# Kernel tuning notes

Measured on AMD Instinct MI355X. Metric: run time of the kernel, lower is better.

## Reference

```python
import jax, jax.numpy as jnp
import numpy as np

N_NODES = 100000
N_EDGES = 8192
DEG = 32                      # nodes per hyperedge
NNZ = N_EDGES * DEG
D_IN = 128
D_HID = 128
D_EDGE = 64
EPS = 1e-5


def _batchnorm(x, g, b):
    # normalize per-feature over the batch (dim 0), as a BatchNorm1d in train mode
    mu = jnp.mean(x, axis=0)
    var = jnp.var(x, axis=0)
    return (x - mu) * jax.lax.rsqrt(var + EPS) * g + b


def _hconv(x, src, eid, w, W, b):
    # hypergraph conv: linear -> node->edge weighted sum -> edge->node weighted sum
    h = x @ W + b                                          # [N, Dout]
    m = jax.ops.segment_sum(w[:, None] * h[src], eid, num_segments=N_EDGES)
    out = jax.ops.segment_sum(w[:, None] * m[eid], src, num_segments=N_NODES)
    return out


def setup_inputs() -> dict:
    key = jax.random.key(0)
    ks = jax.random.split(key, 20)
    src = jax.random.randint(ks[0], (NNZ,), 0, N_NODES)
    eid = jnp.arange(NNZ) // DEG                          # every edge id appears DEG times
    edge_index = jnp.stack([src, eid]).astype(jnp.int64)
    s = lambda k, sh, f: jax.random.normal(k, sh, jnp.float32) * f
    return {
        "x": s(ks[1], (N_NODES, D_IN), 1.0),
        "edge_index": edge_index,
        "edge_weight": jax.random.uniform(ks[2], (NNZ,), jnp.float32),
        "edge_features": s(ks[3], (N_EDGES, D_EDGE), 1.0),
        "adj": jax.random.uniform(ks[4], (N_EDGES, N_EDGES), jnp.float32) / N_EDGES,
        "T": 2,
        "norm1_g": jnp.ones((D_IN,), jnp.float32),
        "norm1_b": jnp.zeros((D_IN,), jnp.float32),
        "norm2_g": jnp.ones((D_EDGE,), jnp.float32),
        "norm2_b": jnp.zeros((D_EDGE,), jnp.float32),
        "W1": s(ks[5], (D_IN, D_HID), 0.05),
        "b1": jnp.zeros((D_HID,), jnp.float32),
        "W2": s(ks[6], (D_HID, D_HID), 0.05),
        "b2": jnp.zeros((D_HID,), jnp.float32),
        "Wn": s(ks[7], (D_HID, D_HID), 0.05),
        "We": s(ks[8], (D_EDGE, D_HID), 0.05),
        "Wg": s(ks[9], (D_HID, D_HID), 0.05),
        "cls_w1": s(ks[10], (D_HID, 16), 0.1),
        "cls_b1": jnp.zeros((16,), jnp.float32),
        "cls_w2": s(ks[11], (16, 2), 0.1),
        "cls_b2": jnp.zeros((2,), jnp.float32),
    }


def reference(x, edge_index, edge_weight, edge_features, adj, T,
              norm1_g, norm1_b, norm2_g, norm2_b,
              W1, b1, W2, b2, Wn, We, Wg,
              cls_w1, cls_b1, cls_w2, cls_b2):
    src, eid = edge_index[0], edge_index[1]
    x = _batchnorm(x, norm1_g, norm1_b)
    x = _hconv(x, src, eid, edge_weight, W1, b1)
    x = _hconv(x, src, eid, edge_weight, W2, b2)
    x = jax.nn.relu(x)
    # aggregate_node_features (mean over nodes incident to each hyperedge) —
    # the per-edge Python loop becomes one fused segment reduce
    s = jax.ops.segment_sum(x[src], eid, num_segments=N_EDGES)           # [E, D]
    cnt = jax.ops.segment_sum(jnp.ones_like(eid, jnp.float32), eid, num_segments=N_EDGES)
    node_features = s / jnp.maximum(cnt, 1.0)[:, None]
    ef = _batchnorm(edge_features, norm2_g, norm2_b)
    # edge-level graph convolution with T propagation steps over edge-edge adj
    h = jax.nn.relu(node_features @ Wn + ef @ We)
    for _ in range(T):
        h = jax.nn.relu(adj @ (h @ Wg))
    # classifier head
    out = jax.nn.relu(h @ cls_w1 + cls_b1) @ cls_w2 + cls_b2             # [E, 2]
    return out
```

## Files before the change

### kernel.cpp

```cpp
#include <hip/hip_runtime.h>

#define N_NODESC 100000
#define N_EDGESC 8192
#define DEGC 32
#define DF 128
#define DEF 64
#define EPSV 1e-5f
#define KSPLIT 8
#define KSLICE (N_EDGESC / KSPLIT)

typedef __attribute__((ext_vector_type(8))) short short8;
typedef __attribute__((ext_vector_type(4))) float f32x4;
typedef __attribute__((ext_vector_type(8))) unsigned short ushort8;
typedef __attribute__((ext_vector_type(4))) unsigned short u16x4;

typedef const void __attribute__((address_space(1)))* gptr_t;
typedef void __attribute__((address_space(3)))* lptr_t;

__device__ __forceinline__ unsigned short f2bf(float x) {
    union { float f; unsigned u; } v; v.f = x;
    unsigned r = v.u + 0x7fffu + ((v.u >> 16) & 1u);
    return (unsigned short)(r >> 16);
}

template<int DCOL, int RP>
__global__ __launch_bounds__(256) void colstats(const float* __restrict__ X, long nrows,
                                                float* __restrict__ stats) {
    const int f = threadIdx.x % DCOL;
    const int rg = threadIdx.x / DCOL;
    float s = 0.f, s2 = 0.f;
    for (long r = (long)blockIdx.x * RP + rg; r < nrows; r += (long)gridDim.x * RP) {
        float v = X[r * DCOL + f];
        s += v; s2 += v * v;
    }
    __shared__ float l1[256], l2[256];
    l1[threadIdx.x] = s; l2[threadIdx.x] = s2;
    __syncthreads();
    if (threadIdx.x < DCOL) {
        for (int g = 1; g < RP; ++g) { s += l1[threadIdx.x + g * DCOL]; s2 += l2[threadIdx.x + g * DCOL]; }
        atomicAdd(&stats[f], s);
        atomicAdd(&stats[DCOL + f], s2);
    }
}

__global__ void finalize_both(const float* __restrict__ stats,
                              const float* __restrict__ g1, const float* __restrict__ b1,
                              const float* __restrict__ g2, const float* __restrict__ b2,
                              float* __restrict__ ssx, float* __restrict__ sse) {
    int t = threadIdx.x;
    if (t < 128) {
        float mean = stats[t] / (float)N_NODESC;
        float var = stats[128 + t] / (float)N_NODESC - mean * mean;
        float sc = g1[t] * rsqrtf(var + EPSV);
        ssx[t] = sc;
        ssx[128 + t] = b1[t] - mean * sc;
    } else {
        int f = t - 128;
        float mean = stats[512 + f] / (float)N_EDGESC;
        float var = stats[576 + f] / (float)N_EDGESC - mean * mean;
        float sc = g2[f] * rsqrtf(var + EPSV);
        sse[f] = sc;
        sse[64 + f] = b2[f] - mean * sc;
    }
}

__global__ __launch_bounds__(256) void csr_fill(const int* __restrict__ src,
                                                const float* __restrict__ ew,
                                                int* __restrict__ cnt,
                                                int* __restrict__ se,
                                                float* __restrict__ swt) {
    int i = blockIdx.x * 256 + threadIdx.x;
    int n = src[i];
    int pos = atomicAdd(&cnt[n], 1);
    if (pos < DEGC) {
        se[(size_t)n * DEGC + pos] = i >> 5;
        swt[(size_t)n * DEGC + pos] = ew[i];
    }
}

__global__ __launch_bounds__(256) void node_apply(const float* __restrict__ m,
                                                  const int* __restrict__ cnt,
                                                  const int* __restrict__ se,
                                                  const float* __restrict__ swt,
                                                  float* __restrict__ out) {
    const int n = blockIdx.x * 2 + (threadIdx.x >> 7);
    const int f = threadIdx.x & 127;
    if (n >= N_NODESC) return;
    int d = cnt[n];
    if (d <= 0) return;
    d = min(d, DEGC);
    const size_t base = (size_t)n * DEGC;
    float acc = 0.f;
    for (int p = 0; p < d; ++p) {
        int e = se[base + p];
        float w = swt[base + p];
        acc += w * m[(size_t)e * DF + f];
    }
    out[(size_t)n * DF + f] = acc;
}

template<bool WEIGHTED, bool AFFINE, bool RELU, bool WRITE_SW>
__global__ __launch_bounds__(128) void gather_k(const float* __restrict__ X,
                                                const float* __restrict__ w,
                                                const int* __restrict__ src,
                                                const float* __restrict__ scale,
                                                const float* __restrict__ shift,
                                                float* __restrict__ out,
                                                float* __restrict__ swout,
                                                float mul) {
    const int e = blockIdx.x, f = threadIdx.x;
    const int base = e * DEGC;
    float acc = 0.f, sw = 0.f;
    #pragma unroll
    for (int j = 0; j < DEGC; ++j) {
        int n = src[base + j];
        float wj = WEIGHTED ? w[base + j] : 1.f;
        float v = X[(size_t)n * DF + f];
        if (RELU) v = fmaxf(v, 0.f);
        acc += wj * v;
        sw += wj;
    }
    float r = acc;
    if (AFFINE) r = acc * scale[f] + sw * shift[f];
    out[(size_t)e * DF + f] = r * mul;
    if (WRITE_SW && f == 0) swout[e] = sw;
}

template<int K1, int K2, int NSLICE, bool RELU_IN, bool RELU_OUT, bool BIAS, bool TBF16>
__global__ __launch_bounds__(256) void egemm(const float* __restrict__ A1, const float* __restrict__ W1p,
                                             const float* __restrict__ A2, const float* __restrict__ W2p,
                                             const float* __restrict__ sc2, const float* __restrict__ sh2,
                                             const float* __restrict__ bias, const float* __restrict__ swv,
                                             float* __restrict__ C, unsigned short* __restrict__ Ct) {
    constexpr int K2c = (K2 > 0) ? K2 : 1;
    constexpr size_t SLSTR = (size_t)N_EDGESC * K1;
    __shared__ float wt1[DF * K1];
    __shared__ float a1c[32 * K1];
    __shared__ float wt2[(K2 > 0) ? DF * K2c : 1];
    __shared__ float a2c[(K2 > 0) ? 32 * K2c : 1];

    const int tid = threadIdx.x;
    const int r0 = blockIdx.x * 32;

    for (int idx = tid; idx < K1 * DF; idx += 256) {
        int k = idx >> 7, c = idx & 127;
        int pc = (k >> 2) ^ ((c >> 3) & 7);
        wt1[c * K1 + pc * 4 + (k & 3)] = W1p[idx];
    }
    for (int idx = tid; idx < 32 * K1; idx += 256) {
        float v;
        if constexpr (NSLICE > 1) {
            v = 0.f;
            #pragma unroll
            for (int s = 0; s < NSLICE; ++s) v += A1[s * SLSTR + (size_t)r0 * K1 + idx];
        } else {
            v = A1[(size_t)r0 * K1 + idx];
        }
        if (RELU_IN) v = fmaxf(v, 0.f);
        a1c[idx] = v;
    }
    if constexpr (K2 > 0) {
        for (int idx = tid; idx < K2 * DF; idx += 256) {
            int k = idx >> 7, c = idx & 127;
            int pc = (k >> 2) ^ ((c >> 3) & 7);
            wt2[c * K2c + pc * 4 + (k & 3)] = W2p[idx];
        }
        for (int idx = tid; idx < 32 * K2; idx += 256) {
            int k = idx % K2;
            a2c[idx] = A2[(size_t)r0 * K2 + idx] * sc2[k] + sh2[k];
        }
    }
    __syncthreads();

    const int cg = tid & 31, rg = tid >> 5;
    const int swz = (cg >> 1) & 7;
    float acc[4][4];
    if constexpr (BIAS) {
        float bl[4], sl[4];
        #pragma unroll
        for (int j = 0; j < 4; ++j) bl[j] = bias[cg * 4 + j];
        #pragma unroll
        for (int i = 0; i < 4; ++i) sl[i] = swv[r0 + rg * 4 + i];
        #pragma unroll
        for (int i = 0; i < 4; ++i)
            #pragma unroll
            for (int j = 0; j < 4; ++j) acc[i][j] = sl[i] * bl[j];
    } else {
        #pragma unroll
        for (int i = 0; i < 4; ++i)
            #pragma unroll
            for (int j = 0; j < 4; ++j) acc[i][j] = 0.f;
    }

    #pragma unroll 4
    for (int k4 = 0; k4 < K1; k4 += 4) {
        f32x4 av[4], wv[4];
        const int pk = (((k4 >> 2) ^ swz) << 2);
        #pragma unroll
        for (int i = 0; i < 4; ++i) av[i] = *(const f32x4*)&a1c[(rg * 4 + i) * K1 + k4];
        #pragma unroll
        for (int j = 0; j < 4; ++j) wv[j] = *(const f32x4*)&wt1[(cg * 4 + j) * K1 + pk];
        #pragma unroll
        for (int i = 0; i < 4; ++i)
            #pragma unroll
            for (int j = 0; j < 4; ++j)
                #pragma unroll
                for (int q = 0; q < 4; ++q) acc[i][j] += av[i][q] * wv[j][q];
    }
    if constexpr (K2 > 0) {
        #pragma unroll 4
        for (int k4 = 0; k4 < K2; k4 += 4) {
            f32x4 av[4], wv[4];
            const int pk = (((k4 >> 2) ^ swz) << 2);
            #pragma unroll
            for (int i = 0; i < 4; ++i) av[i] = *(const f32x4*)&a2c[(rg * 4 + i) * K2c + k4];
            #pragma unroll
            for (int j = 0; j < 4; ++j) wv[j] = *(const f32x4*)&wt2[(cg * 4 + j) * K2c + pk];
            #pragma unroll
            for (int i = 0; i < 4; ++i)
                #pragma unroll
                for (int j = 0; j < 4; ++j)
                    #pragma unroll
                    for (int q = 0; q < 4; ++q) acc[i][j] += av[i][q] * wv[j][q];
        }
    }

    if constexpr (TBF16) {
        #pragma unroll
        for (int j = 0; j < 4; ++j) {
            u16x4 o;
            #pragma unroll
            for (int i = 0; i < 4; ++i) {
                float v = acc[i][j];
                if (RELU_OUT) v = fmaxf(v, 0.f);
                o[i] = f2bf(v);
            }
            *(u16x4*)&Ct[(size_t)(cg * 4 + j) * N_EDGESC + r0 + rg * 4] = o;
        }
    } else {
        #pragma unroll
        for (int i = 0; i < 4; ++i) {
            f32x4 o;
            #pragma unroll
            for (int j = 0; j < 4; ++j) {
                float v = acc[i][j];
                if (RELU_OUT) v = fmaxf(v, 0.f);
                o[j] = v;
            }
            *(f32x4*)&C[(size_t)(r0 + rg * 4 + i) * DF + cg * 4] = o;
        }
    }
}

template<bool CVT>
__global__ __launch_bounds__(256, 2) void adj_gemm(const unsigned short* __restrict__ Abf,
                                                   const float* __restrict__ Af32,
                                                   unsigned short* __restrict__ Aout,
                                                   const unsigned short* __restrict__ Bt,
                                                   float* __restrict__ H) {
    __shared__ unsigned short sA[2][128 * 64];
    __shared__ unsigned short sB[2][128 * 64];
    const int tid = threadIdx.x;
    const int lane = tid & 63, wave = tid >> 6;
    const int mb = blockIdx.x & 63, ks = blockIdx.x >> 6;
    const size_t m0 = (size_t)mb * 128;
    const int k0 = ks * KSLICE;
    const int wm = wave >> 1, wn = wave & 1;
    float* __restrict__ Hs = H + (size_t)ks * (N_EDGESC * DF);

    f32x4 acc[4][4];
    #pragma unroll
    for (int i = 0; i < 4; ++i)
        #pragma unroll
        for (int j = 0; j < 4; ++j) acc[i][j] = 0.f;

    auto stage = [&](int buf, int kc) {
        #pragma unroll
        for (int i = 0; i < 4; ++i) {
            int slot = i * 256 + wave * 64 + lane;
            int row = slot >> 3, ch = slot & 7;
            int sc = (ch ^ (row & 7)) << 3;
            if constexpr (CVT) {
                const float* ga = Af32 + (m0 + row) * (size_t)N_EDGESC + kc + sc;
                f32x4 a = *(const f32x4*)ga;
                f32x4 b = *(const f32x4*)(ga + 4);
                ushort8 r;
                r[0] = f2bf(a[0]); r[1] = f2bf(a[1]); r[2] = f2bf(a[2]); r[3] = f2bf(a[3]);
                r[4] = f2bf(b[0]); r[5] = f2bf(b[1]); r[6] = f2bf(b[2]); r[7] = f2bf(b[3]);
                *(ushort8*)&sA[buf][slot * 8] = r;
                *(ushort8*)(Aout + (m0 + row) * (size_t)N_EDGESC + kc + sc) = r;
            } else {
                const unsigned short* ga = Abf + (m0 + row) * (size_t)N_EDGESC + kc + sc;
                unsigned short* la = &sA[buf][(i * 256 + wave * 64) * 8];
                __builtin_amdgcn_global_load_lds((gptr_t)ga, (lptr_t)la, 16, 0, 0);
            }
            const unsigned short* gb = Bt + (size_t)row * N_EDGESC + kc + sc;
            unsigned short* lb = &sB[buf][(i * 256 + wave * 64) * 8];
            __builtin_amdgcn_global_load_lds((gptr_t)gb, (lptr_t)lb, 16, 0, 0);
        }
    };

    stage(0, k0);
    int cur = 0;
    for (int c = 0; c < KSLICE / 64; ++c) {
        __syncthreads();
        if (c + 1 < KSLICE / 64) stage(cur ^ 1, k0 + (c + 1) * 64);
        #pragma unroll
        for (int kk = 0; kk < 2; ++kk) {
            short8 af[4], bv[4];
            const int chb = kk * 4 + (lane >> 4);
            #pragma unroll
            for (int mf = 0; mf < 4; ++mf) {
                int row = wm * 64 + mf * 16 + (lane & 15);
                af[mf] = *(const short8*)&sA[cur][(row * 8 + (chb ^ (row & 7))) * 8];
            }
            #pragma unroll
            for (int nf = 0; nf < 4; ++nf) {
                int row = wn * 64 + nf * 16 + (lane & 15);
                bv[nf] = *(const short8*)&sB[cur][(row * 8 + (chb ^ (row & 7))) * 8];
            }
            #pragma unroll
            for (int mf = 0; mf < 4; ++mf)
                #pragma unroll
                for (int nf = 0; nf < 4; ++nf)
                    acc[mf][nf] = __builtin_amdgcn_mfma_f32_16x16x32_bf16(af[mf], bv[nf], acc[mf][nf], 0, 0, 0);
        }
        cur ^= 1;
    }

    #pragma unroll
    for (int mf = 0; mf < 4; ++mf)
        #pragma unroll
        for (int nf = 0; nf < 4; ++nf)
            #pragma unroll
            for (int r = 0; r < 4; ++r) {
                size_t row = m0 + wm * 64 + mf * 16 + (lane >> 4) * 4 + r;
                int col = wn * 64 + nf * 16 + (lane & 15);
                Hs[row * DF + col] = acc[mf][nf][r];
            }
}

__global__ __launch_bounds__(256) void classifier_k(const float* __restrict__ H,
                                                    const float* __restrict__ w1, const float* __restrict__ b1,
                                                    const float* __restrict__ w2, const float* __restrict__ b2,
                                                    float* __restrict__ out) {
    constexpr size_t SLSTR = (size_t)N_EDGESC * DF;
    __shared__ float hl[16 * DF];
    __shared__ float w1l[DF * 16];
    __shared__ float hid[16 * 16];
    const int tid = threadIdx.x;
    const int e0 = blockIdx.x * 16;
    for (int idx = tid; idx < 16 * DF; idx += 256) {
        float v = 0.f;
        #pragma unroll
        for (int s = 0; s < KSPLIT; ++s) v += H[s * SLSTR + (size_t)e0 * DF + idx];
        hl[idx] = fmaxf(v, 0.f);
    }
    for (int idx = tid; idx < DF * 16; idx += 256) w1l[idx] = w1[idx];
    __syncthreads();
    {
        int el = tid >> 4, j = tid & 15;
        float a = b1[j];
        for (int k = 0; k < DF; ++k) a += hl[el * DF + k] * w1l[k * 16 + j];
        hid[el * 16 + j] = fmaxf(a, 0.f);
    }
    __syncthreads();
    if (tid < 32) {
        int e = tid >> 1, o = tid & 1;
        float s = b2[o];
        for (int jj = 0; jj < 16; ++jj) s += hid[e * 16 + jj] * w2[jj * 2 + o];
        out[(size_t)(e0 + e) * 2 + o] = s;
    }
}

extern "C" void kernel_launch(void* const* d_in, const int* in_sizes, int n_in,
                              void* d_out, int out_size, void* d_ws, size_t ws_size,
                              hipStream_t stream) {
    const float* x   = (const float*)d_in[0];
    const int*  src  = (const int*)d_in[1];
    const float* ew  = (const float*)d_in[2];
    const float* ef  = (const float*)d_in[3];
    const float* adj = (const float*)d_in[4];
    const float* n1g = (const float*)d_in[6];
    const float* n1b = (const float*)d_in[7];
    const float* n2g = (const float*)d_in[8];
    const float* n2b = (const float*)d_in[9];
    const float* W1  = (const float*)d_in[10];
    const float* b1  = (const float*)d_in[11];
    const float* W2  = (const float*)d_in[12];
    const float* b2  = (const float*)d_in[13];
    const float* Wn  = (const float*)d_in[14];
    const float* We  = (const float*)d_in[15];
    const float* Wg  = (const float*)d_in[16];
    const float* cw1 = (const float*)d_in[17];
    const float* cb1 = (const float*)d_in[18];
    const float* cw2 = (const float*)d_in[19];
    const float* cb2 = (const float*)d_in[20];
    float* out = (float*)d_out;

    float* stats  = (float*)d_ws;
    float* ssx    = stats + 256;
    float* sse    = stats + 640;
    float* sw     = stats + 1024;
    int*   cnt    = (int*)(sw + 8192);
    int*   se     = cnt + N_NODESC;
    float* swt    = (float*)(se + (size_t)N_NODESC * DEGC);
    float* EB0    = swt + (size_t)N_NODESC * DEGC;
    float* EB1    = EB0 + (size_t)N_EDGESC * DF;
    float* HS     = EB1 + (size_t)N_EDGESC * DF;
    float* NODES  = HS + (size_t)KSPLIT * N_EDGESC * DF;
    unsigned short* yT    = (unsigned short*)(NODES + (size_t)N_NODESC * DF);
    unsigned short* adjbf = yT + (size_t)DF * N_EDGESC;

    (void)hipMemsetAsync(stats, 0, (1024 + 8192) * sizeof(float) + N_NODESC * sizeof(int), stream);

    colstats<128, 2><<<400, 256, 0, stream>>>(x, N_NODESC, stats);
    colstats<64, 4><<<64, 256, 0, stream>>>(ef, N_EDGESC, stats + 512);
    finalize_both<<<1, 192, 0, stream>>>(stats, n1g, n1b, n2g, n2b, ssx, sse);

    csr_fill<<<(N_EDGESC * DEGC) / 256, 256, 0, stream>>>(src, ew, cnt, se, swt);

    gather_k<true, true, false, true><<<N_EDGESC, 128, 0, stream>>>(x, ew, src, ssx, ssx + 128, EB0, sw, 1.f);
    egemm<128, 0, 1, false, false, true, false><<<256, 256, 0, stream>>>(EB0, W1, nullptr, nullptr, nullptr, nullptr, b1, sw, EB1, nullptr);
    node_apply<<<N_NODESC / 2, 256, 0, stream>>>(EB1, cnt, se, swt, NODES);

    gather_k<true, false, false, false><<<N_EDGESC, 128, 0, stream>>>(NODES, ew, src, nullptr, nullptr, EB0, nullptr, 1.f);
    egemm<128, 0, 1, false, false, true, false><<<256, 256, 0, stream>>>(EB0, W2, nullptr, nullptr, nullptr, nullptr, b2, sw, EB1, nullptr);
    node_apply<<<N_NODESC / 2, 256, 0, stream>>>(EB1, cnt, se, swt, NODES);

    gather_k<false, false, true, false><<<N_EDGESC, 128, 0, stream>>>(NODES, nullptr, src, nullptr, nullptr, EB0, nullptr, 1.f / DEGC);

    egemm<128, 64, 1, false, true, false, false><<<256, 256, 0, stream>>>(EB0, Wn, ef, We, sse, sse + 64, nullptr, nullptr, EB1, nullptr);

    egemm<128, 0, 1, false, false, false, true><<<256, 256, 0, stream>>>(EB1, Wg, nullptr, nullptr, nullptr, nullptr, nullptr, nullptr, nullptr, yT);
    adj_gemm<true><<<64 * KSPLIT, 256, 0, stream>>>(nullptr, adj, adjbf, yT, HS);
    egemm<128, 0, KSPLIT, true, false, false, true><<<256, 256, 0, stream>>>(HS, Wg, nullptr, nullptr, nullptr, nullptr, nullptr, nullptr, nullptr, yT);
    adj_gemm<false><<<64 * KSPLIT, 256, 0, stream>>>(adjbf, nullptr, nullptr, yT, HS);

    classifier_k<<<N_EDGESC / 16, 256, 0, stream>>>(HS, cw1, cb1, cw2, cb2, out);
}
```

Measured before the change: 546.9 us.

## Read fp32 adj directly in both adj GEMMs with register-prefetched conversion

Both adjacency GEMMs now read the fp32 adj matrix directly. The first pass no longer writes a bf16 copy and the second no longer reads that copy. The A-tile load is split into a register prefetch issued before the MFMA loop and a packed bf16 conversion (v_cvt_pk_bf16_f32) written to LDS after the MFMAs, so global latency overlaps compute. This removes the 128MB bf16 write but doubles the second pass's A reads (256MB fp32 instead of 128MB bf16), and the 32 extra prefetch registers could hurt occupancy.

```diff
diff --git a/kernel.cpp b/kernel.cpp
--- a/kernel.cpp
+++ b/kernel.cpp
@@ -13,6 +13,7 @@
 typedef __attribute__((ext_vector_type(4))) float f32x4;
 typedef __attribute__((ext_vector_type(8))) unsigned short ushort8;
 typedef __attribute__((ext_vector_type(4))) unsigned short u16x4;
+typedef __attribute__((ext_vector_type(4))) unsigned u32x4;
 
 typedef const void __attribute__((address_space(1)))* gptr_t;
 typedef void __attribute__((address_space(3)))* lptr_t;
@@ -21,6 +22,12 @@
     union { float f; unsigned u; } v; v.f = x;
     unsigned r = v.u + 0x7fffu + ((v.u >> 16) & 1u);
     return (unsigned short)(r >> 16);
+}
+
+__device__ __forceinline__ unsigned cvt_pk_bf16(float lo, float hi) {
+    unsigned r;
+    asm("v_cvt_pk_bf16_f32 %0, %1, %2" : "=v"(r) : "v"(lo), "v"(hi));
+    return r;
 }
 
 template<int DCOL, int RP>
@@ -252,10 +259,7 @@
     }
 }
 
-template<bool CVT>
-__global__ __launch_bounds__(256, 2) void adj_gemm(const unsigned short* __restrict__ Abf,
-                                                   const float* __restrict__ Af32,
-                                                   unsigned short* __restrict__ Aout,
+__global__ __launch_bounds__(256, 2) void adj_gemm(const float* __restrict__ Af32,
                                                    const unsigned short* __restrict__ Bt,
                                                    float* __restrict__ H) {
     __shared__ unsigned short sA[2][128 * 64];
@@ -266,6 +270,7 @@
     const size_t m0 = (size_t)mb * 128;
     const int k0 = ks * KSLICE;
     const int wm = wave >> 1, wn = wave & 1;
+    constexpr int NC = KSLICE / 64;
     float* __restrict__ Hs = H + (size_t)ks * (N_EDGESC * DF);
 
     f32x4 acc[4][4];
@@ -274,37 +279,50 @@
         #pragma unroll
         for (int j = 0; j < 4; ++j) acc[i][j] = 0.f;
 
-    auto stage = [&](int buf, int kc) {
+    f32x4 ra[8];
+    auto load_a = [&](int kc) {
         #pragma unroll
         for (int i = 0; i < 4; ++i) {
-            int slot = i * 256 + wave * 64 + lane;
+            int slot = i * 256 + tid;
             int row = slot >> 3, ch = slot & 7;
             int sc = (ch ^ (row & 7)) << 3;
-            if constexpr (CVT) {
-                const float* ga = Af32 + (m0 + row) * (size_t)N_EDGESC + kc + sc;
-                f32x4 a = *(const f32x4*)ga;
-                f32x4 b = *(const f32x4*)(ga + 4);
-                ushort8 r;
-                r[0] = f2bf(a[0]); r[1] = f2bf(a[1]); r[2] = f2bf(a[2]); r[3] = f2bf(a[3]);
-                r[4] = f2bf(b[0]); r[5] = f2bf(b[1]); r[6] = f2bf(b[2]); r[7] = f2bf(b[3]);
-                *(ushort8*)&sA[buf][slot * 8] = r;
-                *(ushort8*)(Aout + (m0 + row) * (size_t)N_EDGESC + kc + sc) = r;
-            } else {
-                const unsigned short* ga = Abf + (m0 + row) * (size_t)N_EDGESC + kc + sc;
-                unsigned short* la = &sA[buf][(i * 256 + wave * 64) * 8];
-                __builtin_amdgcn_global_load_lds((gptr_t)ga, (lptr_t)la, 16, 0, 0);
-            }
+            const float* ga = Af32 + (m0 + row) * (size_t)N_EDGESC + kc + sc;
+            ra[2 * i]     = *(const f32x4*)ga;
+            ra[2 * i + 1] = *(const f32x4*)(ga + 4);
+        }
+    };
+    auto load_b = [&](int buf, int kc) {
+        #pragma unroll
+        for (int i = 0; i < 4; ++i) {
+            int slot = i * 256 + tid;
+            int row = slot >> 3, ch = slot & 7;
+            int sc = (ch ^ (row & 7)) << 3;
             const unsigned short* gb = Bt + (size_t)row * N_EDGESC + kc + sc;
             unsigned short* lb = &sB[buf][(i * 256 + wave * 64) * 8];
             __builtin_amdgcn_global_load_lds((gptr_t)gb, (lptr_t)lb, 16, 0, 0);
         }
     };
-
-    stage(0, k0);
+    auto cvt_write_a = [&](int buf) {
+        #pragma unroll
+        for (int i = 0; i < 4; ++i) {
+            int slot = i * 256 + tid;
+            f32x4 a = ra[2 * i], b = ra[2 * i + 1];
+            u32x4 r;
+            r[0] = cvt_pk_bf16(a[0], a[1]);
+            r[1] = cvt_pk_bf16(a[2], a[3]);
+            r[2] = cvt_pk_bf16(b[0], b[1]);
+            r[3] = cvt_pk_bf16(b[2], b[3]);
+            *(u32x4*)&sA[buf][slot * 8] = r;
+        }
+    };
+
+    load_a(k0);
+    load_b(0, k0);
+    cvt_write_a(0);
     int cur = 0;
-    for (int c = 0; c < KSLICE / 64; ++c) {
+    for (int c = 0; c < NC; ++c) {
         __syncthreads();
-        if (c + 1 < KSLICE / 64) stage(cur ^ 1, k0 + (c + 1) * 64);
+        if (c + 1 < NC) { load_a(k0 + (c + 1) * 64); load_b(cur ^ 1, k0 + (c + 1) * 64); }
         #pragma unroll
         for (int kk = 0; kk < 2; ++kk) {
             short8 af[4], bv[4];
@@ -325,6 +343,7 @@
                 for (int nf = 0; nf < 4; ++nf)
                     acc[mf][nf] = __builtin_amdgcn_mfma_f32_16x16x32_bf16(af[mf], bv[nf], acc[mf][nf], 0, 0, 0);
         }
+        if (c + 1 < NC) cvt_write_a(cur ^ 1);
         cur ^= 1;
     }
 
@@ -409,8 +428,7 @@
     float* EB1    = EB0 + (size_t)N_EDGESC * DF;
     float* HS     = EB1 + (size_t)N_EDGESC * DF;
     float* NODES  = HS + (size_t)KSPLIT * N_EDGESC * DF;
-    unsigned short* yT    = (unsigned short*)(NODES + (size_t)N_NODESC * DF);
-    unsigned short* adjbf = yT + (size_t)DF * N_EDGESC;
+    unsigned short* yT = (unsigned short*)(NODES + (size_t)N_NODESC * DF);
 
     (void)hipMemsetAsync(stats, 0, (1024 + 8192) * sizeof(float) + N_NODESC * sizeof(int), stream);
 
@@ -433,9 +451,9 @@
     egemm<128, 64, 1, false, true, false, false><<<256, 256, 0, stream>>>(EB0, Wn, ef, We, sse, sse + 64, nullptr, nullptr, EB1, nullptr);
 
     egemm<128, 0, 1, false, false, false, true><<<256, 256, 0, stream>>>(EB1, Wg, nullptr, nullptr, nullptr, nullptr, nullptr, nullptr, nullptr, yT);
-    adj_gemm<true><<<64 * KSPLIT, 256, 0, stream>>>(nullptr, adj, adjbf, yT, HS);
+    adj_gemm<<<64 * KSPLIT, 256, 0, stream>>>(adj, yT, HS);
     egemm<128, 0, KSPLIT, true, false, false, true><<<256, 256, 0, stream>>>(HS, Wg, nullptr, nullptr, nullptr, nullptr, nullptr, nullptr, nullptr, yT);
-    adj_gemm<false><<<64 * KSPLIT, 256, 0, stream>>>(adjbf, nullptr, nullptr, yT, HS);
+    adj_gemm<<<64 * KSPLIT, 256, 0, stream>>>(adj, yT, HS);
 
     classifier_k<<<N_EDGESC / 16, 256, 0, stream>>>(HS, cw1, cb1, cw2, cb2, out);
 }
```

Result: no change. 554.2 us (+1.3%).

## Fuse edge-to-node scatter into next gather and pack CSR entries

Applied to the files above, without the earlier changes.

Removes the node_apply kernels and the 100k x 128 NODES buffer. A new gather_sq kernel recomputes each incident node's value on the fly from the per-node (edge, weight) lists while gathering for each hyperedge. CSR edge ids and weights are packed into one struct, and the adj-to-bf16 conversion moves out of the first adj_gemm into a separate kernel. This saves writing and reading the large node buffer, but each node's sum is now recomputed about DEG times, which adds many more random reads of the edge matrix and more arithmetic.

```diff
diff --git a/kernel.cpp b/kernel.cpp
--- a/kernel.cpp
+++ b/kernel.cpp
@@ -16,6 +16,8 @@
 
 typedef const void __attribute__((address_space(1)))* gptr_t;
 typedef void __attribute__((address_space(3)))* lptr_t;
+
+struct EW { int e; float w; };
 
 __device__ __forceinline__ unsigned short f2bf(float x) {
     union { float f; unsigned u; } v; v.f = x;
@@ -64,39 +66,28 @@
     }
 }
 
+__global__ __launch_bounds__(256) void cvt_bf16_k(const float* __restrict__ in,
+                                                  unsigned short* __restrict__ o) {
+    size_t i = (size_t)blockIdx.x * 256 + threadIdx.x;
+    const f32x4* p = (const f32x4*)in + i * 2;
+    f32x4 a = p[0], b = p[1];
+    ushort8 r;
+    r[0] = f2bf(a[0]); r[1] = f2bf(a[1]); r[2] = f2bf(a[2]); r[3] = f2bf(a[3]);
+    r[4] = f2bf(b[0]); r[5] = f2bf(b[1]); r[6] = f2bf(b[2]); r[7] = f2bf(b[3]);
+    *((ushort8*)o + i) = r;
+}
+
 __global__ __launch_bounds__(256) void csr_fill(const int* __restrict__ src,
                                                 const float* __restrict__ ew,
                                                 int* __restrict__ cnt,
-                                                int* __restrict__ se,
-                                                float* __restrict__ swt) {
+                                                EW* __restrict__ ewpk) {
     int i = blockIdx.x * 256 + threadIdx.x;
     int n = src[i];
     int pos = atomicAdd(&cnt[n], 1);
     if (pos < DEGC) {
-        se[(size_t)n * DEGC + pos] = i >> 5;
-        swt[(size_t)n * DEGC + pos] = ew[i];
-    }
-}
-
-__global__ __launch_bounds__(256) void node_apply(const float* __restrict__ m,
-                                                  const int* __restrict__ cnt,
-                                                  const int* __restrict__ se,
-                                                  const float* __restrict__ swt,
-                                                  float* __restrict__ out) {
-    const int n = blockIdx.x * 2 + (threadIdx.x >> 7);
-    const int f = threadIdx.x & 127;
-    if (n >= N_NODESC) return;
-    int d = cnt[n];
-    if (d <= 0) return;
-    d = min(d, DEGC);
-    const size_t base = (size_t)n * DEGC;
-    float acc = 0.f;
-    for (int p = 0; p < d; ++p) {
-        int e = se[base + p];
-        float w = swt[base + p];
-        acc += w * m[(size_t)e * DF + f];
-    }
-    out[(size_t)n * DF + f] = acc;
+        EW t; t.e = i >> 5; t.w = ew[i];
+        ewpk[(size_t)n * DEGC + pos] = t;
+    }
 }
 
 template<bool WEIGHTED, bool AFFINE, bool RELU, bool WRITE_SW>
@@ -126,6 +117,32 @@
     if (WRITE_SW && f == 0) swout[e] = sw;
 }
 
+template<bool RELUMEAN>
+__global__ __launch_bounds__(128) void gather_sq(const float* __restrict__ M,
+                                                 const float* __restrict__ w,
+                                                 const int* __restrict__ src,
+                                                 const int* __restrict__ cnt,
+                                                 const EW* __restrict__ ewpk,
+                                                 float* __restrict__ out, float mul) {
+    const int e = blockIdx.x, f = threadIdx.x;
+    const int base = e * DEGC;
+    float acc = 0.f;
+    #pragma unroll 4
+    for (int j = 0; j < DEGC; ++j) {
+        int n = src[base + j];
+        int d = min(cnt[n], DEGC);
+        const EW* q = ewpk + (size_t)n * DEGC;
+        float xv = 0.f;
+        for (int p = 0; p < d; ++p) {
+            EW t = q[p];
+            xv += t.w * M[(size_t)t.e * DF + f];
+        }
+        if (RELUMEAN) acc += fmaxf(xv, 0.f);
+        else acc += w[base + j] * xv;
+    }
+    out[(size_t)e * DF + f] = acc * mul;
+}
+
 template<int K1, int K2, int NSLICE, bool RELU_IN, bool RELU_OUT, bool BIAS, bool TBF16>
 __global__ __launch_bounds__(256) void egemm(const float* __restrict__ A1, const float* __restrict__ W1p,
                                              const float* __restrict__ A2, const float* __restrict__ W2p,
@@ -252,10 +269,7 @@
     }
 }
 
-template<bool CVT>
-__global__ __launch_bounds__(256, 2) void adj_gemm(const unsigned short* __restrict__ Abf,
-                                                   const float* __restrict__ Af32,
-                                                   unsigned short* __restrict__ Aout,
+__global__ __launch_bounds__(256, 2) void adj_gemm(const unsigned short* __restrict__ A,
                                                    const unsigned short* __restrict__ Bt,
                                                    float* __restrict__ H) {
     __shared__ unsigned short sA[2][128 * 64];
@@ -280,22 +294,11 @@
             int slot = i * 256 + wave * 64 + lane;
             int row = slot >> 3, ch = slot & 7;
             int sc = (ch ^ (row & 7)) << 3;
-            if constexpr (CVT) {
-                const float* ga = Af32 + (m0 + row) * (size_t)N_EDGESC + kc + sc;
-                f32x4 a = *(const f32x4*)ga;
-                f32x4 b = *(const f32x4*)(ga + 4);
-                ushort8 r;
-                r[0] = f2bf(a[0]); r[1] = f2bf(a[1]); r[2] = f2bf(a[2]); r[3] = f2bf(a[3]);
-                r[4] = f2bf(b[0]); r[5] = f2bf(b[1]); r[6] = f2bf(b[2]); r[7] = f2bf(b[3]);
-                *(ushort8*)&sA[buf][slot * 8] = r;
-                *(ushort8*)(Aout + (m0 + row) * (size_t)N_EDGESC + kc + sc) = r;
-            } else {
-                const unsigned short* ga = Abf + (m0 + row) * (size_t)N_EDGESC + kc + sc;
-                unsigned short* la = &sA[buf][(i * 256 + wave * 64) * 8];
-                __builtin_amdgcn_global_load_lds((gptr_t)ga, (lptr_t)la, 16, 0, 0);
-            }
+            const unsigned short* ga = A + (m0 + row) * (size_t)N_EDGESC + kc + sc;
             const unsigned short* gb = Bt + (size_t)row * N_EDGESC + kc + sc;
+            unsigned short* la = &sA[buf][(i * 256 + wave * 64) * 8];
             unsigned short* lb = &sB[buf][(i * 256 + wave * 64) * 8];
+            __builtin_amdgcn_global_load_lds((gptr_t)ga, (lptr_t)la, 16, 0, 0);
             __builtin_amdgcn_global_load_lds((gptr_t)gb, (lptr_t)lb, 16, 0, 0);
         }
     };
@@ -403,13 +406,11 @@
     float* sse    = stats + 640;
     float* sw     = stats + 1024;
     int*   cnt    = (int*)(sw + 8192);
-    int*   se     = cnt + N_NODESC;
-    float* swt    = (float*)(se + (size_t)N_NODESC * DEGC);
-    float* EB0    = swt + (size_t)N_NODESC * DEGC;
+    EW*    ewpk   = (EW*)(cnt + N_NODESC);
+    float* EB0    = (float*)(ewpk + (size_t)N_NODESC * DEGC);
     float* EB1    = EB0 + (size_t)N_EDGESC * DF;
     float* HS     = EB1 + (size_t)N_EDGESC * DF;
-    float* NODES  = HS + (size_t)KSPLIT * N_EDGESC * DF;
-    unsigned short* yT    = (unsigned short*)(NODES + (size_t)N_NODESC * DF);
+    unsigned short* yT    = (unsigned short*)(HS + (size_t)KSPLIT * N_EDGESC * DF);
     unsigned short* adjbf = yT + (size_t)DF * N_EDGESC;
 
     (void)hipMemsetAsync(stats, 0, (1024 + 8192) * sizeof(float) + N_NODESC * sizeof(int), stream);
@@ -418,24 +419,24 @@
     colstats<64, 4><<<64, 256, 0, stream>>>(ef, N_EDGESC, stats + 512);
     finalize_both<<<1, 192, 0, stream>>>(stats, n1g, n1b, n2g, n2b, ssx, sse);
 
-    csr_fill<<<(N_EDGESC * DEGC) / 256, 256, 0, stream>>>(src, ew, cnt, se, swt);
+    csr_fill<<<(N_EDGESC * DEGC) / 256, 256, 0, stream>>>(src, ew, cnt, ewpk);
+
+    cvt_bf16_k<<<(N_EDGESC * (N_EDGESC / 8)) / 256, 256, 0, stream>>>(adj, adjbf);
 
     gather_k<true, true, false, true><<<N_EDGESC, 128, 0, stream>>>(x, ew, src, ssx, ssx + 128, EB0, sw, 1.f);
     egemm<128, 0, 1, false, false, true, false><<<256, 256, 0, stream>>>(EB0, W1, nullptr, nullptr, nullptr, nullptr, b1, sw, EB1, nullptr);
-    node_apply<<<N_NODESC / 2, 256, 0, stream>>>(EB1, cnt, se, swt, NODES);
-
-    gather_k<true, false, false, false><<<N_EDGESC, 128, 0, stream>>>(NODES, ew, src, nullptr, nullptr, EB0, nullptr, 1.f);
+
+    gather_sq<false><<<N_EDGESC, 128, 0, stream>>>(EB1, ew, src, cnt, ewpk, EB0, 1.f);
     egemm<128, 0, 1, false, false, true, false><<<256, 256, 0, stream>>>(EB0, W2, nullptr, nullptr, nullptr, nullptr, b2, sw, EB1, nullptr);
-    node_apply<<<N_NODESC / 2, 256, 0, stream>>>(EB1, cnt, se, swt, NODES);
-
-    gather_k<false, false, true, false><<<N_EDGESC, 128, 0, stream>>>(NODES, nullptr, src, nullptr, nullptr, EB0, nullptr, 1.f / DEGC);
+
+    gather_sq<true><<<N_EDGESC, 128, 0, stream>>>(EB1, nullptr, src, cnt, ewpk, EB0, 1.f / DEGC);
 
     egemm<128, 64, 1, false, true, false, false><<<256, 256, 0, stream>>>(EB0, Wn, ef, We, sse, sse + 64, nullptr, nullptr, EB1, nullptr);
 
     egemm<128, 0, 1, false, false, false, true><<<256, 256, 0, stream>>>(EB1, Wg, nullptr, nullptr, nullptr, nullptr, nullptr, nullptr, nullptr, yT);
-    adj_gemm<true><<<64 * KSPLIT, 256, 0, stream>>>(nullptr, adj, adjbf, yT, HS);
+    adj_gemm<<<64 * KSPLIT, 256, 0, stream>>>(adjbf, yT, HS);
     egemm<128, 0, KSPLIT, true, false, false, true><<<256, 256, 0, stream>>>(HS, Wg, nullptr, nullptr, nullptr, nullptr, nullptr, nullptr, nullptr, yT);
-    adj_gemm<false><<<64 * KSPLIT, 256, 0, stream>>>(adjbf, nullptr, nullptr, yT, HS);
+    adj_gemm<<<64 * KSPLIT, 256, 0, stream>>>(adjbf, yT, HS);
 
     classifier_k<<<N_EDGESC / 16, 256, 0, stream>>>(HS, cw1, cb1, cw2, cb2, out);
 }
```

Result: slower. 572.7 us (+4.7%).
